# Kernel optimization log

Hardware: AMD Instinct MI355X
Metric: run time of the kernel (lower is better)

## Reference

```python
import jax, jax.numpy as jnp
import numpy as np

# Model config (mirrors init_kwargs)
N_HEADS = 32
N_KV_HEADS = 8
HEAD_DIM = 128
DIM = 4096
FREQ_BASE = 500000.0
MAX_SEQ_LEN = 8192
B = 16
T = 16


def _ggml_rope(x, pos):
    """ggml-style RoPE (mode 0): rotates adjacent pairs (x[2i], x[2i+1]).
    x: [B, T, H, HEAD_DIM], pos: [T] int."""
    half = HEAD_DIM // 2
    inv_freq = FREQ_BASE ** (-(jnp.arange(half, dtype=jnp.float32) * 2.0) / HEAD_DIM)  # [half]
    ang = pos.astype(jnp.float32)[:, None] * inv_freq[None, :]                        # [T, half]
    cos = jnp.cos(ang)[None, :, None, :]  # [1, T, 1, half]
    sin = jnp.sin(ang)[None, :, None, :]
    xr = x.reshape(*x.shape[:-1], half, 2)
    x0, x1 = xr[..., 0], xr[..., 1]
    o0 = x0 * cos - x1 * sin
    o1 = x0 * sin + x1 * cos
    return jnp.stack([o0, o1], axis=-1).reshape(x.shape)


def setup_inputs() -> dict:
    key = jax.random.key(0)
    ks = jax.random.split(key, 10)
    x = jax.random.normal(ks[0], (B, T, DIM), dtype=jnp.float32)
    # decode step at the end of the cache -> kv_len == MAX_SEQ_LEN (static)
    input_pos = jnp.arange(MAX_SEQ_LEN - T, MAX_SEQ_LEN, dtype=jnp.int32)
    # causal mask over the full cache: query i may attend to positions <= input_pos[i]
    js = jnp.arange(MAX_SEQ_LEN)
    attn_mask = jnp.where(js[None, :] <= input_pos[:, None], 0.0, -jnp.inf).astype(jnp.float32)  # [T, kv_len]
    k_cache = jax.random.normal(ks[1], (B, MAX_SEQ_LEN, N_KV_HEADS, HEAD_DIM), dtype=jnp.float32)
    v_cache = jax.random.normal(ks[2], (B, MAX_SEQ_LEN, N_KV_HEADS, HEAD_DIM), dtype=jnp.float32)
    s = 1.0 / np.sqrt(DIM)
    wq = jax.random.normal(ks[3], (N_HEADS * HEAD_DIM, DIM), dtype=jnp.float32) * s
    wk = jax.random.normal(ks[4], (N_KV_HEADS * HEAD_DIM, DIM), dtype=jnp.float32) * s
    wv = jax.random.normal(ks[5], (N_KV_HEADS * HEAD_DIM, DIM), dtype=jnp.float32) * s
    wo = jax.random.normal(ks[6], (DIM, N_HEADS * HEAD_DIM), dtype=jnp.float32) * s
    # freqs_cos/freqs_sin are in the torch forward signature but unused (ggml.rope
    # recomputes them from input_pos + freq_base); kept as dummy inputs.
    half = HEAD_DIM // 2
    freqs_cos = jax.random.uniform(ks[7], (T, half), dtype=jnp.float32)
    freqs_sin = jax.random.uniform(ks[8], (T, half), dtype=jnp.float32)
    return {"x": x, "freqs_cos": freqs_cos, "freqs_sin": freqs_sin,
            "input_pos": input_pos, "attn_mask": attn_mask,
            "k_cache": k_cache, "v_cache": v_cache,
            "wq": wq, "wk": wk, "wv": wv, "wo": wo}


def reference(x, freqs_cos, freqs_sin, input_pos, attn_mask, k_cache, v_cache, wq, wk, wv, wo):
    Bx, Tx, _ = x.shape
    n_rep = N_HEADS // N_KV_HEADS
    q = jnp.einsum('btd,ed->bte', x, wq).reshape(Bx, Tx, N_HEADS, HEAD_DIM)
    k = jnp.einsum('btd,ed->bte', x, wk).reshape(Bx, Tx, N_KV_HEADS, HEAD_DIM)
    v = jnp.einsum('btd,ed->bte', x, wv).reshape(Bx, Tx, N_KV_HEADS, HEAD_DIM)
    q = _ggml_rope(q, input_pos)
    k = _ggml_rope(k, input_pos)
    # KV-cache index_copy along time axis
    k_cache = k_cache.at[:, input_pos].set(k)
    v_cache = v_cache.at[:, input_pos].set(v)
    # kv_len = input_pos[0] + T == MAX_SEQ_LEN here (static), so use full cache.
    kq = k_cache  # [B, S, Hkv, D]
    vq = v_cache
    scale = 1.0 / np.sqrt(HEAD_DIM)
    # GQA: group q heads as [g=n_kv, r=n_rep]; equivalent to repeat_interleave on K/V
    qg = q.reshape(Bx, Tx, N_KV_HEADS, n_rep, HEAD_DIM)
    scores = jnp.einsum('btgrd,bsgd->bgrts', qg, kq) * scale  # [B, g, r, T, S]
    scores = scores + attn_mask  # [T, S] broadcasts
    attn = jax.nn.softmax(scores, axis=-1)
    y = jnp.einsum('bgrts,bsgd->btgrd', attn, vq).reshape(Bx, Tx, N_HEADS * HEAD_DIM)
    return jnp.einsum('bte,de->btd', y, wo)
```

## Files before the change

kernel.cpp:

```cpp
#include <hip/hip_runtime.h>
#include <math.h>

#define SEQ 8192
#define NEWBASE 8176
#define NS 4

typedef short s16x4 __attribute__((ext_vector_type(4)));
typedef short s16x8 __attribute__((ext_vector_type(8)));
typedef float f32x4 __attribute__((ext_vector_type(4)));

__device__ __forceinline__ short f2bf(float f) {
  unsigned u = __float_as_uint(f);
  u += 0x7FFFu + ((u >> 16) & 1u);
  return (short)(u >> 16);
}

__device__ __forceinline__ f32x4 mfma16(s16x8 a, s16x8 b, f32x4 c) {
  return __builtin_amdgcn_mfma_f32_16x16x32_bf16(a, b, c, 0, 0, 0);
}

__device__ __forceinline__ void sync_nodrain() {
  __builtin_amdgcn_sched_barrier(0);
  asm volatile("s_waitcnt lgkmcnt(0)" ::: "memory");
  __builtin_amdgcn_s_barrier();
  __builtin_amdgcn_sched_barrier(0);
}

__global__ void rope_table(const int* __restrict__ ipos,
                           float* __restrict__ ctab, float* __restrict__ stab) {
  int i = blockIdx.x * 64 + threadIdx.x;
  int t = i >> 6, f = i & 63;
  double inv = exp(-((double)(2 * f) / 128.0) * log(500000.0));
  double ang = (double)ipos[t] * inv;
  ctab[i] = (float)cos(ang);
  stab[i] = (float)sin(ang);
}

template<int KSTEPS>
__device__ __forceinline__
void gemm_tile(const float* __restrict__ A, const float* __restrict__ Bw,
               float* __restrict__ Cp, int ldc) {
  __shared__ short As[64 * 72];
  __shared__ short Bs[128 * 72];
  const int tid = threadIdx.x, lane = tid & 63, w = tid >> 6;
  const int l15 = lane & 15, l4 = lane >> 4;
  f32x4 acc[8] = {};
  float4 ar[4], br[8];

  auto issue = [&](int st) {
    const float* Ab = A + st * 64;
    const float* Bb = Bw + st * 64;
#pragma unroll
    for (int i = 0; i < 4; ++i) {
      int id = tid + i * 256;
      ar[i] = *(const float4*)(Ab + (size_t)(id >> 4) * 4096 + ((id & 15) << 2));
    }
#pragma unroll
    for (int i = 0; i < 8; ++i) {
      int id = tid + i * 256;
      br[i] = *(const float4*)(Bb + (size_t)(id >> 4) * 4096 + ((id & 15) << 2));
    }
  };

  issue(0);
  for (int st = 0; st < KSTEPS; ++st) {
#pragma unroll
    for (int i = 0; i < 4; ++i) {
      int id = tid + i * 256, row = id >> 4, c4 = (id & 15) << 2;
      s16x4 h = { f2bf(ar[i].x), f2bf(ar[i].y), f2bf(ar[i].z), f2bf(ar[i].w) };
      *(s16x4*)&As[row * 72 + c4] = h;
    }
#pragma unroll
    for (int i = 0; i < 8; ++i) {
      int id = tid + i * 256, row = id >> 4, c4 = (id & 15) << 2;
      s16x4 h = { f2bf(br[i].x), f2bf(br[i].y), f2bf(br[i].z), f2bf(br[i].w) };
      *(s16x4*)&Bs[row * 72 + c4] = h;
    }
    sync_nodrain();
    if (st + 1 < KSTEPS) issue(st + 1);
    __builtin_amdgcn_sched_barrier(0);
#pragma unroll
    for (int kk = 0; kk < 64; kk += 32) {
      s16x8 a = *(const s16x8*)&As[(w * 16 + l15) * 72 + kk + l4 * 8];
#pragma unroll
      for (int nf = 0; nf < 8; ++nf) {
        s16x8 b = *(const s16x8*)&Bs[(nf * 16 + l15) * 72 + kk + l4 * 8];
        acc[nf] = mfma16(a, b, acc[nf]);
      }
    }
    sync_nodrain();
  }
#pragma unroll
  for (int nf = 0; nf < 8; ++nf)
#pragma unroll
    for (int r = 0; r < 4; ++r)
      Cp[(size_t)(w * 16 + l4 * 4 + r) * ldc + nf * 16 + l15] = acc[nf][r];
}

__global__ __launch_bounds__(256)
__attribute__((amdgpu_waves_per_eu(4, 4)))
void gemm_qkv(const float* __restrict__ x,
              const float* __restrict__ wq, const float* __restrict__ wk,
              const float* __restrict__ wv, float* __restrict__ part) {
  int bn = blockIdx.x, bm = blockIdx.y, sp = blockIdx.z;
  const float* Bw;
  if (bn < 32)      Bw = wq + (size_t)(bn * 128) * 4096;
  else if (bn < 40) Bw = wk + (size_t)((bn - 32) * 128) * 4096;
  else              Bw = wv + (size_t)((bn - 40) * 128) * 4096;
  const float* A = x + (size_t)(bm * 64) * 4096 + sp * 1024;
  float* Cp = part + (size_t)sp * (256 * 6144) + (size_t)(bm * 64) * 6144 + bn * 128;
  gemm_tile<16>(A, Bw + sp * 1024, Cp, 6144);
}

__global__ __launch_bounds__(256)
__attribute__((amdgpu_waves_per_eu(4, 4)))
void gemm_out(const float* __restrict__ y, const float* __restrict__ wo,
              float* __restrict__ part) {
  int bn = blockIdx.x, bm = blockIdx.y, sp = blockIdx.z;
  const float* A = y + (size_t)(bm * 64) * 4096 + sp * 1024;
  const float* Bw = wo + (size_t)(bn * 128) * 4096 + sp * 1024;
  float* Cp = part + (size_t)sp * (256 * 4096) + (size_t)(bm * 64) * 4096 + bn * 128;
  gemm_tile<16>(A, Bw, Cp, 4096);
}

__global__ __launch_bounds__(256)
void rope_reduce(const float* __restrict__ part, const float* __restrict__ ctab,
                 const float* __restrict__ stab, float* __restrict__ q,
                 float* __restrict__ kn, float* __restrict__ vn) {
  int idx = blockIdx.x * 256 + threadIdx.x;
  int m = idx / 3072;
  int col = (idx - m * 3072) * 2;
  const float* src = part + (size_t)m * 6144 + col;
  float a0 = 0.f, a1 = 0.f;
#pragma unroll
  for (int s = 0; s < 4; ++s) {
    a0 += src[(size_t)s * 1572864];
    a1 += src[(size_t)s * 1572864 + 1];
  }
  if (col < 5120) {
    int local = (col < 4096) ? col : col - 4096;
    int f = (local & 127) >> 1, t = m & 15;
    float c = ctab[t * 64 + f], sn = stab[t * 64 + f];
    float o0 = a0 * c - a1 * sn, o1 = a0 * sn + a1 * c;
    if (col < 4096) {
      q[(size_t)m * 4096 + col] = o0;
      q[(size_t)m * 4096 + col + 1] = o1;
    } else {
      kn[(size_t)m * 1024 + local] = o0;
      kn[(size_t)m * 1024 + local + 1] = o1;
    }
  } else {
    int local = col - 5120;
    vn[(size_t)m * 1024 + local] = a0;
    vn[(size_t)m * 1024 + local + 1] = a1;
  }
}

__global__ __launch_bounds__(512)
__attribute__((amdgpu_waves_per_eu(4, 4)))
void attn4(const float* __restrict__ kc_, const float* __restrict__ vc_,
           const float* __restrict__ qb, const float* __restrict__ kn,
           const float* __restrict__ vn, const int* __restrict__ ipos,
           float* __restrict__ pO, float* __restrict__ pM, float* __restrict__ pL) {
  __shared__ short Ks[2][32 * 128];
  __shared__ short Vt[2][128 * 34];
  __shared__ short Ps[4 * 16 * 40];
  const int sh = blockIdx.x, g = blockIdx.y, b = blockIdx.z;
  const int tid = threadIdx.x, lane = tid & 63, w = tid >> 6;
  const int l15 = lane & 15, l4 = lane >> 4;
  const float scale = 0.08838834764831845f;
  const int sbase = sh * 2048;

  const float* kc_b = kc_ + (size_t)b * SEQ * 1024 + g * 128;
  const float* vc_b = vc_ + (size_t)b * SEQ * 1024 + g * 128;
  const float* kn_b = kn + (size_t)b * 16 * 1024 + g * 128;
  const float* vn_b = vn + (size_t)b * 16 * 1024 + g * 128;

  if (w < 4) {
    const int krow = tid >> 5, kc4 = (tid & 31) << 2;
    const int vcol = tid & 127, vhr = (tid >> 7) << 4;
    float4 kA[4], kB[4];
    float vA[16], vB[16];

    auto issue = [&](int cb, float4 (&kr)[4], float (&vr)[16]) {
      if (cb + 32 <= NEWBASE) {
#pragma unroll
        for (int i = 0; i < 4; ++i)
          kr[i] = *(const float4*)(kc_b + (size_t)(cb + krow + i * 8) * 1024 + kc4);
#pragma unroll
        for (int j = 0; j < 16; ++j)
          vr[j] = vc_b[(size_t)(cb + vhr + j) * 1024 + vcol];
      } else {
#pragma unroll
        for (int i = 0; i < 4; ++i) {
          int sg = cb + krow + i * 8;
          const float* src = (sg >= NEWBASE)
              ? (kn_b + (size_t)(sg - NEWBASE) * 1024 + kc4)
              : (kc_b + (size_t)sg * 1024 + kc4);
          kr[i] = *(const float4*)src;
        }
#pragma unroll
        for (int j = 0; j < 16; ++j) {
          int sg = cb + vhr + j;
          vr[j] = (sg >= NEWBASE)
              ? vn_b[(size_t)(sg - NEWBASE) * 1024 + vcol]
              : vc_b[(size_t)sg * 1024 + vcol];
        }
      }
    };
    auto convert = [&](int buf, const float4 (&kr)[4], const float (&vr)[16]) {
#pragma unroll
      for (int i = 0; i < 4; ++i) {
        int s = krow + i * 8;
        s16x4 hv = { f2bf(kr[i].x), f2bf(kr[i].y), f2bf(kr[i].z), f2bf(kr[i].w) };
        *(s16x4*)&Ks[buf][s * 128 + (kc4 ^ ((s & 7) << 3))] = hv;
      }
#pragma unroll
      for (int j4 = 0; j4 < 4; ++j4) {
        s16x4 hv = { f2bf(vr[j4 * 4]), f2bf(vr[j4 * 4 + 1]),
                     f2bf(vr[j4 * 4 + 2]), f2bf(vr[j4 * 4 + 3]) };
        *(s16x4*)&Vt[buf][vcol * 34 + vhr + j4 * 4] = hv;
      }
    };

    issue(sbase, kA, vA);
    issue(sbase + 32, kB, vB);
    convert(0, kA, vA);
    sync_nodrain();
    for (int c = 1; c < 64; c += 2) {
      convert(1, kB, vB);
      if (c + 1 < 64) issue(sbase + (c + 1) * 32, kA, vA);
      sync_nodrain();
      if (c + 1 < 64) convert(0, kA, vA);
      if (c + 2 < 64) issue(sbase + (c + 2) * 32, kB, vB);
      sync_nodrain();
    }
  } else {
    const int qg = w - 4;
    s16x8 qa[4];
    {
      int qr = qg * 16 + l15;
      int t = qr >> 2, r = qr & 3, h = g * 4 + r;
      const float* qp = qb + (size_t)(b * 16 + t) * 4096 + h * 128;
#pragma unroll
      for (int ks = 0; ks < 4; ++ks) {
        float4 v0 = *(const float4*)(qp + ks * 32 + l4 * 8);
        float4 v1 = *(const float4*)(qp + ks * 32 + l4 * 8 + 4);
        qa[ks] = s16x8{ f2bf(v0.x), f2bf(v0.y), f2bf(v0.z), f2bf(v0.w),
                        f2bf(v1.x), f2bf(v1.y), f2bf(v1.z), f2bf(v1.w) };
      }
    }
    const int ip_t = ipos[qg * 4 + l4];
    f32x4 o[8] = {};
    float mrun[4] = { -1e30f, -1e30f, -1e30f, -1e30f };
    float lrun[4] = { 0.f, 0.f, 0.f, 0.f };
    short* Pw = &Ps[qg * (16 * 40)];

    sync_nodrain();
    for (int c = 0; c < 64; ++c) {
      const short* Kb = &Ks[c & 1][0];
      const short* Vb = &Vt[c & 1][0];
      const int base = sbase + c * 32;
      f32x4 sc[2] = {};
#pragma unroll
      for (int ks = 0; ks < 4; ++ks) {
        int dd = ks * 32 + l4 * 8;
#pragma unroll
        for (int nf = 0; nf < 2; ++nf) {
          int s = nf * 16 + l15;
          s16x8 kb = *(const s16x8*)&Kb[s * 128 + (dd ^ ((s & 7) << 3))];
          sc[nf] = mfma16(qa[ks], kb, sc[nf]);
        }
      }
      float cmax[4] = { -1e30f, -1e30f, -1e30f, -1e30f };
#pragma unroll
      for (int nf = 0; nf < 2; ++nf) {
        int sg = base + nf * 16 + l15;
#pragma unroll
        for (int r = 0; r < 4; ++r) {
          float v = sc[nf][r] * scale;
          v = (sg <= ip_t) ? v : -1e30f;
          sc[nf][r] = v;
          cmax[r] = fmaxf(cmax[r], v);
        }
      }
#pragma unroll
      for (int r = 0; r < 4; ++r) {
        cmax[r] = fmaxf(cmax[r], __shfl_xor(cmax[r], 1, 64));
        cmax[r] = fmaxf(cmax[r], __shfl_xor(cmax[r], 2, 64));
        cmax[r] = fmaxf(cmax[r], __shfl_xor(cmax[r], 4, 64));
        cmax[r] = fmaxf(cmax[r], __shfl_xor(cmax[r], 8, 64));
      }
      bool grow = (cmax[0] > mrun[0]) | (cmax[1] > mrun[1]) |
                  (cmax[2] > mrun[2]) | (cmax[3] > mrun[3]);
      if (__any(grow)) {
#pragma unroll
        for (int r = 0; r < 4; ++r) {
          float mn = fmaxf(mrun[r], cmax[r]);
          float cf = __expf(mrun[r] - mn);
          mrun[r] = mn;
          lrun[r] *= cf;
#pragma unroll
          for (int nd = 0; nd < 8; ++nd) o[nd][r] *= cf;
        }
      }
      float rsum[4] = { 0.f, 0.f, 0.f, 0.f };
#pragma unroll
      for (int nf = 0; nf < 2; ++nf) {
#pragma unroll
        for (int r = 0; r < 4; ++r) {
          float p = __expf(sc[nf][r] - mrun[r]);
          rsum[r] += p;
          Pw[(l4 * 4 + r) * 40 + nf * 16 + l15] = f2bf(p);
        }
      }
#pragma unroll
      for (int r = 0; r < 4; ++r) {
        rsum[r] += __shfl_xor(rsum[r], 1, 64);
        rsum[r] += __shfl_xor(rsum[r], 2, 64);
        rsum[r] += __shfl_xor(rsum[r], 4, 64);
        rsum[r] += __shfl_xor(rsum[r], 8, 64);
        lrun[r] += rsum[r];
      }
      s16x8 pa = *(const s16x8*)&Pw[l15 * 40 + l4 * 8];
#pragma unroll
      for (int nd = 0; nd < 8; ++nd) {
        int d = nd * 16 + l15;
        s16x8 vb = *(const s16x8*)&Vb[d * 34 + l4 * 8];
        o[nd] = mfma16(pa, vb, o[nd]);
      }
      sync_nodrain();
    }
    const int blk = (b * 8 + g) * NS + sh;
    float* Ob = pO + (size_t)blk * 64 * 128;
#pragma unroll
    for (int nd = 0; nd < 8; ++nd)
#pragma unroll
      for (int r = 0; r < 4; ++r)
        Ob[(qg * 16 + l4 * 4 + r) * 128 + nd * 16 + l15] = o[nd][r];
    if (l15 == 0) {
#pragma unroll
      for (int r = 0; r < 4; ++r) {
        pM[blk * 64 + qg * 16 + l4 * 4 + r] = mrun[r];
        pL[blk * 64 + qg * 16 + l4 * 4 + r] = lrun[r];
      }
    }
  }
}

__global__ __launch_bounds__(256)
void merge(const float* __restrict__ pO, const float* __restrict__ pM,
           const float* __restrict__ pL, float* __restrict__ y) {
  const int g = blockIdx.x, b = blockIdx.y;
  const int bb = (b * 8 + g) * NS;
#pragma unroll 4
  for (int i = 0; i < 32; ++i) {
    int id = threadIdx.x + i * 256;
    int qr = id >> 7, d = id & 127;
    float M = -1e30f;
    for (int p = 0; p < NS; ++p) M = fmaxf(M, pM[(bb + p) * 64 + qr]);
    float acc = 0.f, den = 0.f;
    for (int p = 0; p < NS; ++p) {
      float a = __expf(pM[(bb + p) * 64 + qr] - M);
      acc += pO[(size_t)(bb + p) * 8192 + id] * a;
      den += pL[(bb + p) * 64 + qr] * a;
    }
    int t = qr >> 2, r = qr & 3, h = g * 4 + r;
    y[(size_t)(b * 16 + t) * 4096 + h * 128 + d] = acc / den;
  }
}

__global__ __launch_bounds__(256)
void out_reduce(const float* __restrict__ part, float* __restrict__ out) {
  int i = blockIdx.x * 256 + threadIdx.x;
  const f32x4* p4 = (const f32x4*)part;
  f32x4 s = {0.f, 0.f, 0.f, 0.f};
#pragma unroll
  for (int sp = 0; sp < 4; ++sp) s += p4[(size_t)sp * 262144 + i];
  ((f32x4*)out)[i] = s;
}

extern "C" void kernel_launch(void* const* d_in, const int* in_sizes, int n_in,
                              void* d_out, int out_size, void* d_ws, size_t ws_size,
                              hipStream_t stream) {
  const float* x      = (const float*)d_in[0];
  const int*   ipos   = (const int*)d_in[3];
  const float* kcache = (const float*)d_in[5];
  const float* vcache = (const float*)d_in[6];
  const float* wq     = (const float*)d_in[7];
  const float* wk     = (const float*)d_in[8];
  const float* wv     = (const float*)d_in[9];
  const float* wo     = (const float*)d_in[10];
  float* out = (float*)d_out;

  float* q_buf = (float*)d_ws;
  float* k_new = q_buf + 1048576;
  float* v_new = k_new + 262144;
  float* y_buf = v_new + 262144;
  float* ctab  = y_buf + 1048576;
  float* stab  = ctab + 1024;
  float* pO    = stab + 1024;
  float* pM    = pO + 8388608;
  float* pL    = pM + 65536;
  float* qkvp  = pO;
  float* outp  = pO;

  rope_table<<<16, 64, 0, stream>>>(ipos, ctab, stab);
  gemm_qkv<<<dim3(48, 4, 4), 256, 0, stream>>>(x, wq, wk, wv, qkvp);
  rope_reduce<<<3072, 256, 0, stream>>>(qkvp, ctab, stab, q_buf, k_new, v_new);
  attn4<<<dim3(NS, 8, 16), 512, 0, stream>>>(kcache, vcache, q_buf, k_new, v_new,
                                             ipos, pO, pM, pL);
  merge<<<dim3(8, 16), 256, 0, stream>>>(pO, pM, pL, y_buf);
  gemm_out<<<dim3(32, 4, 4), 256, 0, stream>>>(y_buf, wo, outp);
  out_reduce<<<1024, 256, 0, stream>>>(outp, out);
}
```

Measured before the change: 349.3 us.

## Quad-buffer K/V shared tiles and process two chunks per barrier

The attention kernel's producer/consumer pipeline now uses four LDS buffers instead of two. The loader converts and stores two chunks per iteration while keeping two chunks of global loads in flight. Compute waves handle two 32-row chunks between barriers, so the number of block-wide syncs is halved. Compute waves also raise their wave priority while doing MFMA work. This doubles the LDS used for K/V, which could limit how many blocks fit per CU.

```diff
diff --git a/kernel.cpp b/kernel.cpp
--- a/kernel.cpp
+++ b/kernel.cpp
@@ -158,12 +158,12 @@
 
 __global__ __launch_bounds__(512)
 __attribute__((amdgpu_waves_per_eu(4, 4)))
-void attn4(const float* __restrict__ kc_, const float* __restrict__ vc_,
+void attn5(const float* __restrict__ kc_, const float* __restrict__ vc_,
            const float* __restrict__ qb, const float* __restrict__ kn,
            const float* __restrict__ vn, const int* __restrict__ ipos,
            float* __restrict__ pO, float* __restrict__ pM, float* __restrict__ pL) {
-  __shared__ short Ks[2][32 * 128];
-  __shared__ short Vt[2][128 * 34];
+  __shared__ short Ks[4][32 * 128];
+  __shared__ short Vt[4][128 * 34];
   __shared__ short Ps[4 * 16 * 40];
   const int sh = blockIdx.x, g = blockIdx.y, b = blockIdx.z;
   const int tid = threadIdx.x, lane = tid & 63, w = tid >> 6;
@@ -208,31 +208,39 @@
         }
       }
     };
-    auto convert = [&](int buf, const float4 (&kr)[4], const float (&vr)[16]) {
+    auto convert = [&](short* Kd, short* Vd,
+                       const float4 (&kr)[4], const float (&vr)[16]) {
 #pragma unroll
       for (int i = 0; i < 4; ++i) {
         int s = krow + i * 8;
         s16x4 hv = { f2bf(kr[i].x), f2bf(kr[i].y), f2bf(kr[i].z), f2bf(kr[i].w) };
-        *(s16x4*)&Ks[buf][s * 128 + (kc4 ^ ((s & 7) << 3))] = hv;
+        *(s16x4*)&Kd[s * 128 + (kc4 ^ ((s & 7) << 3))] = hv;
       }
 #pragma unroll
       for (int j4 = 0; j4 < 4; ++j4) {
         s16x4 hv = { f2bf(vr[j4 * 4]), f2bf(vr[j4 * 4 + 1]),
                      f2bf(vr[j4 * 4 + 2]), f2bf(vr[j4 * 4 + 3]) };
-        *(s16x4*)&Vt[buf][vcol * 34 + vhr + j4 * 4] = hv;
+        *(s16x4*)&Vd[vcol * 34 + vhr + j4 * 4] = hv;
       }
     };
 
     issue(sbase, kA, vA);
     issue(sbase + 32, kB, vB);
-    convert(0, kA, vA);
+    convert(Ks[0], Vt[0], kA, vA);
+    issue(sbase + 64, kA, vA);
+    convert(Ks[1], Vt[1], kB, vB);
+    issue(sbase + 96, kB, vB);
     sync_nodrain();
-    for (int c = 1; c < 64; c += 2) {
-      convert(1, kB, vB);
-      if (c + 1 < 64) issue(sbase + (c + 1) * 32, kA, vA);
-      sync_nodrain();
-      if (c + 1 < 64) convert(0, kA, vA);
-      if (c + 2 < 64) issue(sbase + (c + 2) * 32, kB, vB);
+    for (int p = 0; p < 32; ++p) {
+      int cA = 2 * p + 2, cB = 2 * p + 3;
+      if (cA < 64) {
+        convert(Ks[cA & 3], Vt[cA & 3], kA, vA);
+        if (cA + 2 < 64) issue(sbase + (cA + 2) * 32, kA, vA);
+      }
+      if (cB < 64) {
+        convert(Ks[cB & 3], Vt[cB & 3], kB, vB);
+        if (cB + 2 < 64) issue(sbase + (cB + 2) * 32, kB, vB);
+      }
       sync_nodrain();
     }
   } else {
@@ -256,10 +264,9 @@
     float lrun[4] = { 0.f, 0.f, 0.f, 0.f };
     short* Pw = &Ps[qg * (16 * 40)];
 
-    sync_nodrain();
-    for (int c = 0; c < 64; ++c) {
-      const short* Kb = &Ks[c & 1][0];
-      const short* Vb = &Vt[c & 1][0];
+    auto compute = [&](int c) {
+      const short* Kb = &Ks[c & 3][0];
+      const short* Vb = &Vt[c & 3][0];
       const int base = sbase + c * 32;
       f32x4 sc[2] = {};
 #pragma unroll
@@ -329,6 +336,14 @@
         s16x8 vb = *(const s16x8*)&Vb[d * 34 + l4 * 8];
         o[nd] = mfma16(pa, vb, o[nd]);
       }
+    };
+
+    sync_nodrain();
+    for (int p = 0; p < 32; ++p) {
+      __builtin_amdgcn_s_setprio(1);
+      compute(2 * p);
+      compute(2 * p + 1);
+      __builtin_amdgcn_s_setprio(0);
       sync_nodrain();
     }
     const int blk = (b * 8 + g) * NS + sh;
@@ -408,7 +423,7 @@
   rope_table<<<16, 64, 0, stream>>>(ipos, ctab, stab);
   gemm_qkv<<<dim3(48, 4, 4), 256, 0, stream>>>(x, wq, wk, wv, qkvp);
   rope_reduce<<<3072, 256, 0, stream>>>(qkvp, ctab, stab, q_buf, k_new, v_new);
-  attn4<<<dim3(NS, 8, 16), 512, 0, stream>>>(kcache, vcache, q_buf, k_new, v_new,
+  attn5<<<dim3(NS, 8, 16), 512, 0, stream>>>(kcache, vcache, q_buf, k_new, v_new,
                                              ipos, pO, pM, pL);
   merge<<<dim3(8, 16), 256, 0, stream>>>(pO, pM, pL, y_buf);
   gemm_out<<<dim3(32, 4, 4), 256, 0, stream>>>(y_buf, wo, outp);
```

After: 384.5 us. +10.1%, slower.
